# Optimization experiments

Measured on AMD Instinct MI355X. Metric: run time of the kernel, lower is better.

Reference implementation:

```python
import jax, jax.numpy as jnp
import numpy as np

TOP_K_PCT = 0.25   # cfg.dsa_top_k_pct
STRIDE = 8         # hardcoded downsample stride in derive_mask
SIGMOID_SHARP = 10.0
NEG_INF = -1e9


def setup_inputs() -> dict:
    key = jax.random.key(0)
    kq, kk, kv, ku = jax.random.split(key, 4)
    B, nH, T, hd = 1, 4, 4096, 128
    Q = jax.random.normal(kq, (B, nH, T, hd), dtype=jnp.float32)
    K = jax.random.normal(kk, (B, nH, T, hd), dtype=jnp.float32)
    V = jax.random.normal(kv, (B, nH, T, hd), dtype=jnp.float32)
    U = jax.random.uniform(ku, (B, T), dtype=jnp.float32)
    return {"Q": Q, "K": K, "V": V, "U": U}


def _derive_mask(Q, K, U):
    B, nH, T, hd = Q.shape
    scale = hd ** -0.5
    # downsampled local attention scores: (B, nH, T//8, T//8)
    Q_ds = Q[:, :, ::STRIDE, :]
    K_ds = K[:, :, ::STRIDE, :]
    scores = jnp.einsum('bhid,bhjd->bhij', Q_ds, K_ds) * scale
    # upsample back to (B, nH, T, T) via nearest-neighbor repeat
    scores_full = jnp.repeat(jnp.repeat(scores, STRIDE, axis=2), STRIDE, axis=3)[:, :, :T, :T]
    # ECT uncertainty weighting: (B, 1, T, 1)
    u_scale = (1.0 + jnp.clip(U, 0.0, 1.0))[:, None, :, None]
    scores_full = scores_full * u_scale
    # per-row k-th largest value == kthvalue(T - k + 1 smallest)
    k = max(1, int(T * TOP_K_PCT))
    threshold_val = jax.lax.top_k(scores_full, k)[0][..., -1:]  # (B, nH, T, 1)
    return jax.nn.sigmoid((scores_full - threshold_val) * SIGMOID_SHARP)


def reference(Q, K, V, U):
    B, nH, T, hd = Q.shape
    scale = hd ** -0.5
    mask = _derive_mask(Q, K, U)
    causal = jnp.tril(jnp.ones((T, T), dtype=bool))
    mask = mask * causal[None, None, :, :]
    scores = jnp.einsum('bhid,bhjd->bhij', Q, K) * scale
    scores = scores + (1.0 - mask) * NEG_INF
    attn = jax.nn.softmax(scores, axis=-1)
    return jnp.einsum('bhij,bhjd->bhid', attn, V)
```

## Files before the change

### kernel.cpp

```cpp
#include <hip/hip_runtime.h>
#include <math.h>

#define T_SEQ 4096
#define HD 128
#define NH 4
#define DS 512
#define SCALE 0.08838834764831845f
#define NEG9 (-1.0e9f)
#define BN 32
#define NCH 128
#define NRT 256
#define SEG 16
#define TOTSEG2 144
#define NVP 32
#define ALIVE_MIN (-999999936.0f)

typedef __attribute__((ext_vector_type(8))) _Float16 half8;
typedef __attribute__((ext_vector_type(4))) float floatx4;

__device__ __forceinline__ float sigmoidf_(float x) {
  if (x >= 0.0f) return 1.0f / (1.0f + expf(-x));
  float e = expf(x);
  return e / (1.0f + e);
}

#define GLDS16(g, l)                                                  \
  __builtin_amdgcn_global_load_lds(                                   \
      (const __attribute__((address_space(1))) void*)(g),             \
      (__attribute__((address_space(3))) void*)(l), 16, 0, 0)

__global__ __launch_bounds__(256) void prepsds_kernel(
    const float* __restrict__ Q, const float* __restrict__ K, const float* __restrict__ V,
    _Float16* __restrict__ KVb, float* __restrict__ Vpart, float* __restrict__ sds) {
  const int bx = blockIdx.x, tid = threadIdx.x;
  __shared__ float tile[32][133];
  __shared__ float red[2][128];
  __shared__ float Qs[16][132];
  __shared__ float Ks[16][132];
  if (bx < 512) {
    const int hh = bx >> 7, c = bx & 127;
    const int j0 = c * 32;
    const int w = tid >> 6, lane = tid & 63;
    const size_t blob = (size_t)(hh * NCH + c) * 12288;
#pragma unroll
    for (int tt = 0; tt < 2; ++tt) {
      const int t = w + tt * 4;
      const int halfj = t >> 2, dd = t & 3;
      const int q = lane >> 4, jm = lane & 15;
      const float* src =
          &K[(size_t)((hh * T_SEQ) + j0 + halfj * 16 + jm) * HD + dd * 32 + q * 8];
      float4 x0 = *(const float4*)src;
      float4 x1 = *(const float4*)(src + 4);
      float v[8] = {x0.x, x0.y, x0.z, x0.w, x1.x, x1.y, x1.z, x1.w};
      half8 oh, oe;
#pragma unroll
      for (int e = 0; e < 8; ++e) {
        _Float16 hv = (_Float16)v[e];
        oh[e] = hv;
        oe[e] = (_Float16)(v[e] - (float)hv);
      }
      const size_t o = blob + ((size_t)t * 64 + lane) * 8;
      *(half8*)&KVb[o] = oh;
      *(half8*)&KVb[o + 4096] = oe;
    }
    for (int k = 0; k < 4; ++k) {
      int row = (tid >> 5) + k * 8;
      int col = (tid & 31) * 4;
      *(float4*)&tile[row][col] =
          *(const float4*)&V[(size_t)((hh * T_SEQ) + j0 + row) * HD + col];
    }
    __syncthreads();
#pragma unroll
    for (int s2 = 0; s2 < 2; ++s2) {
      const int o8 = tid + s2 * 256;
      const int t2 = o8 >> 6, lane2 = o8 & 63;
      const int qa = lane2 >> 4, dl = lane2 & 15;
      const int col = (t2 >> 1) * 32 + (t2 & 1) * 16 + dl;
      half8 v8;
#pragma unroll
      for (int e = 0; e < 8; ++e) {
        const int row = (e < 4) ? (qa * 4 + e) : (16 + qa * 4 + (e - 4));
        v8[e] = (_Float16)tile[row][col];
      }
      *(half8*)&KVb[blob + 8192 + (size_t)o8 * 8] = v8;
    }
  } else if (bx < 640) {
    int b = bx - 512;
    int hh = b >> 5, part = b & 31;
    int d = tid & 127, hlf = tid >> 7;
    const int j0 = part * 128 + hlf;
    float s0 = 0.f, s1 = 0.f;
    for (int j = j0; j < part * 128 + 128; j += 4) {
      s0 += V[(size_t)((hh * T_SEQ) + j) * HD + d];
      s1 += V[(size_t)((hh * T_SEQ) + j + 2) * HD + d];
    }
    red[hlf][d] = s0 + s1;
    __syncthreads();
    if (tid < 128)
      Vpart[(hh * NVP + part) * 128 + tid] = red[0][tid] + red[1][tid];
  } else {
    int b = bx - 640;
    const int bxs = b & 31, bys = (b >> 5) & 31, hh = b >> 10;
    for (int t = tid; t < 512; t += 256) {
      int r = t >> 5, f = (t & 31) * 4;
      *(float4*)&Qs[r][f] = *(const float4*)&Q[((hh * T_SEQ) + (bys * 16 + r) * 8) * HD + f];
      *(float4*)&Ks[r][f] = *(const float4*)&K[((hh * T_SEQ) + (bxs * 16 + r) * 8) * HD + f];
    }
    __syncthreads();
    const int ty = tid >> 4, tx = tid & 15;
    float acc = 0.0f;
    for (int k = 0; k < 32; ++k) {
      float4 a = *(float4*)&Qs[ty][k * 4];
      float4 bq = *(float4*)&Ks[tx][k * 4];
      acc += a.x * bq.x + a.y * bq.y + a.z * bq.z + a.w * bq.w;
    }
    sds[((hh * DS) + bys * 16 + ty) * DS + bxs * 16 + tx] = acc * SCALE;
  }
}

__global__ __launch_bounds__(256) void bmaxthr_kernel(const float* __restrict__ sds,
                                                      const float* __restrict__ U,
                                                      float* __restrict__ thrG,
                                                      float* __restrict__ bmax16) {
  const int h = blockIdx.y, rt = blockIdx.x;
  const int tid = threadIdx.x, ww = tid >> 6, lane = tid & 63;
  __shared__ float thrS[2];
  if (ww < 2) {
    const int row = h * DS + rt * 2 + ww;
    unsigned v[8];
    for (int t = 0; t < 8; ++t) {
      float f = sds[(size_t)row * DS + t * 64 + lane];
      unsigned b = __float_as_uint(f);
      v[t] = (b & 0x80000000u) ? ~b : (b | 0x80000000u);
    }
    unsigned prefix = 0u;
    for (int bit = 31; bit >= 0; --bit) {
      unsigned cand = prefix | (1u << bit);
      int c = 0;
      for (int t = 0; t < 8; ++t) c += (v[t] >= cand) ? 1 : 0;
      for (int off = 32; off > 0; off >>= 1) c += __shfl_down(c, off, 64);
      c = __shfl(c, 0, 64);
      if (c >= 128) prefix = cand;
    }
    if (lane == 0) {
      unsigned b = (prefix & 0x80000000u) ? (prefix ^ 0x80000000u) : ~prefix;
      float t = __uint_as_float(b);
      thrS[ww] = t;
      thrG[row] = t;
    }
  }
  __syncthreads();
  const int r = lane >> 2, q = lane & 3;
  const int i = rt * 16 + r;
  float u = U[i];
  u = fminf(fmaxf(u, 0.0f), 1.0f);
  const float us = 1.0f + u;
  const int idl = r >> 3;
  const float bb = us * thrS[idl];
  const float* srow = &sds[((h * DS) + rt * 2 + idl) * DS];
  for (int c = ww; c < NCH; c += 4) {
    float sval = srow[(c << 2) + q];
    float a = us * sval;
    float bias = (1.0f - sigmoidf_((a - bb) * 10.0f)) * NEG9;
    for (int off = 1; off < 64; off <<= 1)
      bias = fmaxf(bias, __shfl_xor(bias, off, 64));
    if (lane == 0) bmax16[((h * NRT) + rt) * NCH + c] = bias;
  }
}

__global__ __launch_bounds__(512) void attn128_kernel(
    const float* __restrict__ Qf, const _Float16* __restrict__ KVb,
    const float* __restrict__ U, const float* __restrict__ sds,
    const float* __restrict__ thrG, const float* __restrict__ bmax16,
    float* __restrict__ Pm, float* __restrict__ Pl, _Float16* __restrict__ Po,
    const float* __restrict__ Vpart, float* __restrict__ out) {
  const int h = blockIdx.y;
  const int p = TOTSEG2 - 1 - (int)blockIdx.x;
  int s = 0;
#pragma unroll
  for (int t = 1; t <= 7; ++t)
    if (p >= 32 * t - 2 * t * (t - 1)) s = t;
  const int g = 4 * s + (p - (32 * s - 2 * s * (s - 1)));
  const int seg = s;
  const int cmax = 4 * g + 4;
  const int c0 = seg * SEG;
  const int len = min(SEG, cmax - c0);
  const int nsegG = (cmax + 15) >> 4;

  const int tid = threadIdx.x;
  const int w = tid >> 6;
  const int lane = tid & 63;
  const int quad = lane >> 4;
  const int n = lane & 15;

  const int rt = g * 8 + w;
  const int iw0 = g * 128 + w * 16;
  const int nchW = (rt >> 1) + 1;

  __shared__ __align__(16) _Float16 Sbuf[2][12288];
  __shared__ unsigned uHot[8], uNN[8];
  __shared__ float VsS[128];

  const int myidn = (iw0 >> 3) + (n >> 3);
  float usn, bbn;
  {
    float u = U[iw0 + n];
    u = fminf(fmaxf(u, 0.0f), 1.0f);
    usn = 1.0f + u;
    bbn = usn * thrG[h * DS + myidn];
  }

  half8 qfh[4], qfe[4];
  {
    const float* qrow = &Qf[(size_t)((h * T_SEQ) + iw0 + n) * HD + quad * 8];
#pragma unroll
    for (int d = 0; d < 4; ++d) {
      float4 x0 = *(const float4*)&qrow[d * 32];
      float4 x1 = *(const float4*)&qrow[d * 32 + 4];
      float v[8] = {x0.x, x0.y, x0.z, x0.w, x1.x, x1.y, x1.z, x1.w};
      half8 hh, ee;
#pragma unroll
      for (int t = 0; t < 8; ++t) {
        _Float16 hv = (_Float16)v[t];
        hh[t] = hv;
        ee[t] = (_Float16)(v[t] - (float)hv);
      }
      qfh[d] = hh;
      qfe[d] = ee;
    }
  }
  half8 vones;
#pragma unroll
  for (int e = 0; e < 8; ++e) vones[e] = (_Float16)1.0f;

  floatx4 acc[8];
  for (int t = 0; t < 8; ++t) acc[t] = (floatx4){0.f, 0.f, 0.f, 0.f};
  floatx4 accL = (floatx4){0.f, 0.f, 0.f, 0.f};
  float m_ = -INFINITY;

  float bval = -3.0e38f;
  bool validc = false;
  if (lane < len) {
    int c = c0 + lane;
    validc = (c < nchW);
    bval = bmax16[((h * NRT) + rt) * NCH + c];
  }
  const unsigned bits = (1u << len) - 1u;
  const unsigned myHot = (unsigned)__ballot(lane < len && validc && bval > -124.0f) & bits;
  const unsigned myNull = (unsigned)__ballot(lane < len && (!validc || bval == NEG9)) & bits;
  const unsigned myCold = bits & ~myHot & ~myNull;
  if (lane == 0) { uHot[w] = myHot; uNN[w] = myHot | myCold; }
  __syncthreads();
  unsigned it0 = uHot[0] | uHot[1] | uHot[2] | uHot[3] |
                 uHot[4] | uHot[5] | uHot[6] | uHot[7];
  unsigned it1 = (uNN[0] | uNN[1] | uNN[2] | uNN[3] |
                  uNN[4] | uNN[5] | uNN[6] | uNN[7]) & ~it0;

  const size_t hcbase = (size_t)(h * NCH);
#define STAGE(cc, bsel)                                                          \
  {                                                                              \
    const _Float16* gsrc =                                                       \
        KVb + (hcbase + (size_t)(c0 + (cc))) * 12288 + w * 1536 + lane * 8;      \
    _Float16* ldst = &Sbuf[bsel][w * 1536];                                      \
    GLDS16(gsrc, ldst);                                                          \
    GLDS16(gsrc + 512, ldst + 512);                                              \
    GLDS16(gsrc + 1024, ldst + 1024);                                            \
  }

  int curc = -1;
  if (it0) { curc = __builtin_ctz(it0); it0 &= it0 - 1; }
  else if (it1) { curc = __builtin_ctz(it1); it1 &= it1 - 1; }
  int cur = 0;
  if (curc >= 0) STAGE(curc, 0);

  while (curc >= 0) {
    __syncthreads();
    int nxtc = -1;
    if (it0) { nxtc = __builtin_ctz(it0); it0 &= it0 - 1; }
    else if (it1) { nxtc = __builtin_ctz(it1); it1 &= it1 - 1; }
    if (nxtc >= 0) STAGE(nxtc, cur ^ 1);

    bool run = ((myHot | myCold) >> curc) & 1;
    if (run && ((myCold >> curc) & 1)) {
      float bm16 = __shfl(bval, curc, 64);
      float mm = m_;
      for (int d = 1; d < 16; d <<= 1) mm = fminf(mm, __shfl_xor(mm, d, 64));
      if (bm16 + 12.0f < mm - 40.0f) run = false;
    }
    if (run) {
      const _Float16* Sb = &Sbuf[cur][0];
      const int c = c0 + curc;
      const int j0 = c * BN;

      const int jj = quad >> 1;
      const float sv1 = sds[((h * DS) + myidn) * DS + (c << 2) + jj];
      const float sv2 = sds[((h * DS) + myidn) * DS + (c << 2) + 2 + jj];
      const float bias1 = (1.0f - sigmoidf_((usn * sv1 - bbn) * 10.0f)) * NEG9;
      const float bias2 = (1.0f - sigmoidf_((usn * sv2 - bbn) * 10.0f)) * NEG9;

      half8 kh0[4], kh1[4];
#pragma unroll
      for (int d = 0; d < 4; ++d) {
        kh0[d] = *(const half8*)&Sb[(size_t)(d * 64 + lane) * 8];
        kh1[d] = *(const half8*)&Sb[(size_t)((4 + d) * 64 + lane) * 8];
      }

      floatx4 S0a = (floatx4){0.f, 0.f, 0.f, 0.f};
      floatx4 S0b = (floatx4){0.f, 0.f, 0.f, 0.f};
      floatx4 S1a = (floatx4){0.f, 0.f, 0.f, 0.f};
      floatx4 S1b = (floatx4){0.f, 0.f, 0.f, 0.f};
      S0a = __builtin_amdgcn_mfma_f32_16x16x32_f16(kh0[0], qfh[0], S0a, 0, 0, 0);
      S0b = __builtin_amdgcn_mfma_f32_16x16x32_f16(kh0[2], qfh[2], S0b, 0, 0, 0);
      S1a = __builtin_amdgcn_mfma_f32_16x16x32_f16(kh1[0], qfh[0], S1a, 0, 0, 0);
      S1b = __builtin_amdgcn_mfma_f32_16x16x32_f16(kh1[2], qfh[2], S1b, 0, 0, 0);
      S0a = __builtin_amdgcn_mfma_f32_16x16x32_f16(kh0[1], qfh[1], S0a, 0, 0, 0);
      S0b = __builtin_amdgcn_mfma_f32_16x16x32_f16(kh0[3], qfh[3], S0b, 0, 0, 0);
      S1a = __builtin_amdgcn_mfma_f32_16x16x32_f16(kh1[1], qfh[1], S1a, 0, 0, 0);
      S1b = __builtin_amdgcn_mfma_f32_16x16x32_f16(kh1[3], qfh[3], S1b, 0, 0, 0);

      S0a = __builtin_amdgcn_mfma_f32_16x16x32_f16(kh0[0], qfe[0], S0a, 0, 0, 0);
      S0b = __builtin_amdgcn_mfma_f32_16x16x32_f16(kh0[2], qfe[2], S0b, 0, 0, 0);
      S1a = __builtin_amdgcn_mfma_f32_16x16x32_f16(kh1[0], qfe[0], S1a, 0, 0, 0);
      S1b = __builtin_amdgcn_mfma_f32_16x16x32_f16(kh1[2], qfe[2], S1b, 0, 0, 0);
      S0a = __builtin_amdgcn_mfma_f32_16x16x32_f16(kh0[1], qfe[1], S0a, 0, 0, 0);
      S0b = __builtin_amdgcn_mfma_f32_16x16x32_f16(kh0[3], qfe[3], S0b, 0, 0, 0);
      S1a = __builtin_amdgcn_mfma_f32_16x16x32_f16(kh1[1], qfe[1], S1a, 0, 0, 0);
      S1b = __builtin_amdgcn_mfma_f32_16x16x32_f16(kh1[3], qfe[3], S1b, 0, 0, 0);

      half8 ke0[4], ke1[4];
#pragma unroll
      for (int d = 0; d < 4; ++d) {
        ke0[d] = *(const half8*)&Sb[4096 + (size_t)(d * 64 + lane) * 8];
        ke1[d] = *(const half8*)&Sb[4096 + (size_t)((4 + d) * 64 + lane) * 8];
      }
      S0a = __builtin_amdgcn_mfma_f32_16x16x32_f16(ke0[0], qfh[0], S0a, 0, 0, 0);
      S0b = __builtin_amdgcn_mfma_f32_16x16x32_f16(ke0[2], qfh[2], S0b, 0, 0, 0);
      S1a = __builtin_amdgcn_mfma_f32_16x16x32_f16(ke1[0], qfh[0], S1a, 0, 0, 0);
      S1b = __builtin_amdgcn_mfma_f32_16x16x32_f16(ke1[2], qfh[2], S1b, 0, 0, 0);
      S0a = __builtin_amdgcn_mfma_f32_16x16x32_f16(ke0[1], qfh[1], S0a, 0, 0, 0);
      S0b = __builtin_amdgcn_mfma_f32_16x16x32_f16(ke0[3], qfh[3], S0b, 0, 0, 0);
      S1a = __builtin_amdgcn_mfma_f32_16x16x32_f16(ke1[1], qfh[1], S1a, 0, 0, 0);
      S1b = __builtin_amdgcn_mfma_f32_16x16x32_f16(ke1[3], qfh[3], S1b, 0, 0, 0);

      const floatx4 S0 = S0a + S0b;
      const floatx4 S1 = S1a + S1b;

      const int i = iw0 + n;
      float sc0[4], sc1[4];
      for (int r = 0; r < 4; ++r) {
        const int jA = j0 + quad * 4 + r;
        sc0[r] = (jA <= i) ? (S0[r] * SCALE + bias1) : NEG9;
        sc1[r] = (jA + 16 <= i) ? (S1[r] * SCALE + bias2) : NEG9;
      }

      bool within = true;
      for (int r = 0; r < 4; ++r)
        within = within && (sc0[r] <= m_ + 8.0f) && (sc1[r] <= m_ + 8.0f);
      _Float16 ph0[4], ph1[4];
      if (__all(within)) {
        for (int r = 0; r < 4; ++r) {
          ph0[r] = (_Float16)__expf(sc0[r] - m_);
          ph1[r] = (_Float16)__expf(sc1[r] - m_);
        }
      } else {
        float mx = sc0[0];
        for (int r = 1; r < 4; ++r) mx = fmaxf(mx, sc0[r]);
        for (int r = 0; r < 4; ++r) mx = fmaxf(mx, sc1[r]);
        mx = fmaxf(mx, __shfl_xor(mx, 16, 64));
        mx = fmaxf(mx, __shfl_xor(mx, 32, 64));
        const float mnew = fmaxf(m_, mx);
        const float alpha = __expf(m_ - mnew);
        for (int r = 0; r < 4; ++r) {
          ph0[r] = (_Float16)__expf(sc0[r] - mnew);
          ph1[r] = (_Float16)__expf(sc1[r] - mnew);
        }
        m_ = mnew;
        if (__any(alpha != 1.0f)) {
          float aO[4];
#pragma unroll
          for (int r = 0; r < 4; ++r) aO[r] = __shfl(alpha, quad * 4 + r, 64);
          for (int t = 0; t < 8; ++t)
            for (int r = 0; r < 4; ++r) acc[t][r] *= aO[r];
          for (int r = 0; r < 4; ++r) accL[r] *= aO[r];
        }
      }

      half8 pp;
#pragma unroll
      for (int r = 0; r < 4; ++r) { pp[r] = ph0[r]; pp[4 + r] = ph1[r]; }

      half8 vf[8];
#pragma unroll
      for (int t = 0; t < 8; ++t)
        vf[t] = *(const half8*)&Sb[8192 + (size_t)(t * 64 + lane) * 8];

#pragma unroll
      for (int t = 0; t < 8; ++t)
        acc[t] = __builtin_amdgcn_mfma_f32_16x16x32_f16(pp, vf[t], acc[t], 0, 0, 0);
      accL = __builtin_amdgcn_mfma_f32_16x16x32_f16(pp, vones, accL, 0, 0, 0);
    }
    cur ^= 1;
    curc = nxtc;
  }

  float mrow[4];
#pragma unroll
  for (int r = 0; r < 4; ++r) mrow[r] = __shfl(m_, quad * 4 + r, 64);

  if (nsegG == 1) {
    if (tid < 128) {
      float ss = 0.f;
      for (int pt = 0; pt < NVP; ++pt) ss += Vpart[(h * NVP + pt) * 128 + tid];
      VsS[tid] = ss;
    }
    __syncthreads();
    for (int r = 0; r < 4; ++r) {
      const int row = iw0 + quad * 4 + r;
      const bool dead = (mrow[r] < ALIVE_MIN);
      const float Linv = dead ? 0.0f : 1.0f / accL[r];
#pragma unroll
      for (int t = 0; t < 8; ++t) {
        const int col = t * 16 + n;
        float o = dead ? VsS[col] * 0.000244140625f : acc[t][r] * Linv;
        out[(size_t)((h * T_SEQ) + row) * HD + col] = o;
      }
    }
    return;
  }
  __syncthreads();
  const size_t pbase = (size_t)(h * TOTSEG2 + p);
  if (quad == 0) Pm[pbase * 128 + w * 16 + n] = m_;
  if (n == 0) {
    for (int r = 0; r < 4; ++r)
      Pl[pbase * 128 + w * 16 + quad * 4 + r] = accL[r];
  }
  _Float16* Ob = &Sbuf[0][0];
#pragma unroll
  for (int t = 0; t < 8; ++t)
    for (int r = 0; r < 4; ++r)
      Ob[(size_t)(w * 16 + quad * 4 + r) * 128 + t * 16 + n] = (_Float16)acc[t][r];
  __syncthreads();
  {
    const half8* Os = (const half8*)Ob;
    half8* Pod = (half8*)&Po[pbase * 16384];
    for (int idx = tid; idx < 2048; idx += 512) Pod[idx] = Os[idx];
  }
}

__global__ __launch_bounds__(256) void reduce128_kernel(const float* __restrict__ Pm,
                                                        const float* __restrict__ Pl,
                                                        const _Float16* __restrict__ Po,
                                                        const float* __restrict__ Vpart,
                                                        float* __restrict__ out) {
  const int bx = blockIdx.x;
  const int g = 4 + (bx >> 3);
  const int rb = bx & 7;
  const int h = blockIdx.y;
  const int ns = (g >> 2) + 1;
  const int tid = threadIdx.x;
  const int lr = tid >> 4;
  const int d0 = (tid & 15) * 8;
  const int r = rb * 16 + lr;

  float m[8], M = -INFINITY;
  int pp[8];
#pragma unroll
  for (int ss = 0; ss < 8; ++ss) {
    if (ss < ns) {
      pp[ss] = 32 * ss - 2 * ss * (ss - 1) + g - 4 * ss;
      m[ss] = Pm[(size_t)(h * TOTSEG2 + pp[ss]) * 128 + r];
      M = fmaxf(M, m[ss]);
    }
  }
  const bool dead = (M < ALIVE_MIN);
  float es[8], L = 0.f;
#pragma unroll
  for (int ss = 0; ss < 8; ++ss) {
    if (ss < ns) {
      es[ss] = (dead || m[ss] == -INFINITY) ? 0.0f : expf(m[ss] - M);
      L += Pl[(size_t)(h * TOTSEG2 + pp[ss]) * 128 + r] * es[ss];
    }
  }

  float o[8];
#pragma unroll
  for (int e = 0; e < 8; ++e) o[e] = 0.f;
  if (dead) {
    float4 sa = {0.f, 0.f, 0.f, 0.f}, sb = {0.f, 0.f, 0.f, 0.f};
    for (int pt = 0; pt < NVP; ++pt) {
      const float* vp = &Vpart[(h * NVP + pt) * 128 + d0];
      float4 x0 = *(const float4*)vp;
      float4 x1 = *(const float4*)(vp + 4);
      sa.x += x0.x; sa.y += x0.y; sa.z += x0.z; sa.w += x0.w;
      sb.x += x1.x; sb.y += x1.y; sb.z += x1.z; sb.w += x1.w;
    }
    o[0] = sa.x * 0.000244140625f; o[1] = sa.y * 0.000244140625f;
    o[2] = sa.z * 0.000244140625f; o[3] = sa.w * 0.000244140625f;
    o[4] = sb.x * 0.000244140625f; o[5] = sb.y * 0.000244140625f;
    o[6] = sb.z * 0.000244140625f; o[7] = sb.w * 0.000244140625f;
  } else {
    const float Linv = 1.0f / L;
#pragma unroll
    for (int ss = 0; ss < 8; ++ss) {
      if (ss < ns) {
        half8 v = *(const half8*)&Po[(size_t)(h * TOTSEG2 + pp[ss]) * 16384 + r * 128 + d0];
#pragma unroll
        for (int e = 0; e < 8; ++e) o[e] += (float)v[e] * es[ss];
      }
    }
#pragma unroll
    for (int e = 0; e < 8; ++e) o[e] *= Linv;
  }
  float* dst = &out[(size_t)((h * T_SEQ) + g * 128 + r) * HD + d0];
  float4 w0 = {o[0], o[1], o[2], o[3]};
  float4 w1 = {o[4], o[5], o[6], o[7]};
  *(float4*)dst = w0;
  *(float4*)(dst + 4) = w1;
}

extern "C" void kernel_launch(void* const* d_in, const int* in_sizes, int n_in,
                              void* d_out, int out_size, void* d_ws, size_t ws_size,
                              hipStream_t stream) {
  const float* Q = (const float*)d_in[0];
  const float* K = (const float*)d_in[1];
  const float* V = (const float*)d_in[2];
  const float* U = (const float*)d_in[3];
  float* out = (float*)d_out;

  char* wsb = (char*)d_ws;
  float* sds = (float*)wsb;
  float* thrG = (float*)(wsb + 4194304);
  float* bmax16 = (float*)(wsb + 4202496);
  float* Vpart = (float*)(wsb + 4726784);
  _Float16* KVb = (_Float16*)(wsb + 4792320);
  float* Pm = (float*)(wsb + 17375232);
  float* Pl = (float*)(wsb + 17670144);
  _Float16* Po = (_Float16*)(wsb + 17965056);

  prepsds_kernel<<<4736, 256, 0, stream>>>(Q, K, V, KVb, Vpart, sds);
  bmaxthr_kernel<<<dim3(NRT, NH), 256, 0, stream>>>(sds, U, thrG, bmax16);
  attn128_kernel<<<dim3(TOTSEG2, NH), 512, 0, stream>>>(Q, KVb, U, sds, thrG, bmax16,
                                                        Pm, Pl, Po, Vpart, out);
  reduce128_kernel<<<dim3(224, NH), 256, 0, stream>>>(Pm, Pl, Po, Vpart, out);
}
```

Measured before the change: 224.3 us.

## Process two 16-row tiles per wavefront in attention kernel with 256 threads

The attention kernel now runs 4 wavefronts per block instead of 8, and each wavefront handles two 16-row query tiles. Every K/V fragment read from LDS therefore feeds MFMAs for both tiles, halving LDS fragment traffic per row and giving more independent MFMAs to interleave. The cost is roughly double the accumulator and Q-fragment registers per wave, which may lower occupancy. Each wave also issues twice as many global-to-LDS loads per stage, and the cold-chunk skip test is now shared across both tiles, so it becomes more conservative.

```diff
diff --git a/kernel.cpp b/kernel.cpp
--- a/kernel.cpp
+++ b/kernel.cpp
@@ -168,7 +168,7 @@
   }
 }
 
-__global__ __launch_bounds__(512) void attn128_kernel(
+__global__ __launch_bounds__(256) void attn128_kernel(
     const float* __restrict__ Qf, const _Float16* __restrict__ KVb,
     const float* __restrict__ U, const float* __restrict__ sds,
     const float* __restrict__ thrG, const float* __restrict__ bmax16,
@@ -193,26 +193,27 @@
   const int quad = lane >> 4;
   const int n = lane & 15;
 
-  const int rt = g * 8 + w;
-  const int iw0 = g * 128 + w * 16;
-  const int nchW = (rt >> 1) + 1;
-
   __shared__ __align__(16) _Float16 Sbuf[2][12288];
-  __shared__ unsigned uHot[8], uNN[8];
+  __shared__ unsigned uHot[4], uNN[4];
   __shared__ float VsS[128];
 
-  const int myidn = (iw0 >> 3) + (n >> 3);
-  float usn, bbn;
-  {
-    float u = U[iw0 + n];
+  int iw0t[2], rtt[2], myid[2];
+  float usn[2], bbn[2];
+#pragma unroll
+  for (int tt = 0; tt < 2; ++tt) {
+    iw0t[tt] = g * 128 + (w * 2 + tt) * 16;
+    rtt[tt] = g * 8 + w * 2 + tt;
+    myid[tt] = (iw0t[tt] >> 3) + (n >> 3);
+    float u = U[iw0t[tt] + n];
     u = fminf(fmaxf(u, 0.0f), 1.0f);
-    usn = 1.0f + u;
-    bbn = usn * thrG[h * DS + myidn];
-  }
-
-  half8 qfh[4], qfe[4];
-  {
-    const float* qrow = &Qf[(size_t)((h * T_SEQ) + iw0 + n) * HD + quad * 8];
+    usn[tt] = 1.0f + u;
+    bbn[tt] = usn[tt] * thrG[h * DS + myid[tt]];
+  }
+
+  half8 qfh[2][4], qfe[2][4];
+#pragma unroll
+  for (int tt = 0; tt < 2; ++tt) {
+    const float* qrow = &Qf[(size_t)((h * T_SEQ) + iw0t[tt] + n) * HD + quad * 8];
 #pragma unroll
     for (int d = 0; d < 4; ++d) {
       float4 x0 = *(const float4*)&qrow[d * 32];
@@ -225,46 +226,59 @@
         hh[t] = hv;
         ee[t] = (_Float16)(v[t] - (float)hv);
       }
-      qfh[d] = hh;
-      qfe[d] = ee;
+      qfh[tt][d] = hh;
+      qfe[tt][d] = ee;
     }
   }
   half8 vones;
 #pragma unroll
   for (int e = 0; e < 8; ++e) vones[e] = (_Float16)1.0f;
 
-  floatx4 acc[8];
-  for (int t = 0; t < 8; ++t) acc[t] = (floatx4){0.f, 0.f, 0.f, 0.f};
-  floatx4 accL = (floatx4){0.f, 0.f, 0.f, 0.f};
-  float m_ = -INFINITY;
-
-  float bval = -3.0e38f;
-  bool validc = false;
+  floatx4 acc[2][8];
+#pragma unroll
+  for (int tt = 0; tt < 2; ++tt)
+    for (int t = 0; t < 8; ++t) acc[tt][t] = (floatx4){0.f, 0.f, 0.f, 0.f};
+  floatx4 accL[2];
+  accL[0] = (floatx4){0.f, 0.f, 0.f, 0.f};
+  accL[1] = (floatx4){0.f, 0.f, 0.f, 0.f};
+  float m_[2] = {-INFINITY, -INFINITY};
+
+  float bv[2] = {-3.0e38f, -3.0e38f};
+  bool hot0 = false, hot1 = false, nul0 = true, nul1 = true;
   if (lane < len) {
     int c = c0 + lane;
-    validc = (c < nchW);
-    bval = bmax16[((h * NRT) + rt) * NCH + c];
-  }
+#pragma unroll
+    for (int tt = 0; tt < 2; ++tt) {
+      bool vd = (c < (rtt[tt] >> 1) + 1);
+      float b = bmax16[((h * NRT) + rtt[tt]) * NCH + c];
+      bv[tt] = b;
+      bool ht = vd && b > -124.0f;
+      bool nl = (!vd) || b == NEG9;
+      if (tt == 0) { hot0 = ht; nul0 = nl; } else { hot1 = ht; nul1 = nl; }
+    }
+  }
+  const float bvalM = fmaxf(bv[0], bv[1]);
   const unsigned bits = (1u << len) - 1u;
-  const unsigned myHot = (unsigned)__ballot(lane < len && validc && bval > -124.0f) & bits;
-  const unsigned myNull = (unsigned)__ballot(lane < len && (!validc || bval == NEG9)) & bits;
+  const unsigned myHot = (unsigned)__ballot(lane < len && (hot0 || hot1)) & bits;
+  const unsigned myNull = (unsigned)__ballot(lane < len && nul0 && nul1) & bits;
   const unsigned myCold = bits & ~myHot & ~myNull;
   if (lane == 0) { uHot[w] = myHot; uNN[w] = myHot | myCold; }
   __syncthreads();
-  unsigned it0 = uHot[0] | uHot[1] | uHot[2] | uHot[3] |
-                 uHot[4] | uHot[5] | uHot[6] | uHot[7];
-  unsigned it1 = (uNN[0] | uNN[1] | uNN[2] | uNN[3] |
-                  uNN[4] | uNN[5] | uNN[6] | uNN[7]) & ~it0;
+  unsigned it0 = uHot[0] | uHot[1] | uHot[2] | uHot[3];
+  unsigned it1 = (uNN[0] | uNN[1] | uNN[2] | uNN[3]) & ~it0;
 
   const size_t hcbase = (size_t)(h * NCH);
 #define STAGE(cc, bsel)                                                          \
   {                                                                              \
     const _Float16* gsrc =                                                       \
-        KVb + (hcbase + (size_t)(c0 + (cc))) * 12288 + w * 1536 + lane * 8;      \
-    _Float16* ldst = &Sbuf[bsel][w * 1536];                                      \
+        KVb + (hcbase + (size_t)(c0 + (cc))) * 12288 + w * 3072 + lane * 8;      \
+    _Float16* ldst = &Sbuf[bsel][w * 3072];                                      \
     GLDS16(gsrc, ldst);                                                          \
     GLDS16(gsrc + 512, ldst + 512);                                              \
     GLDS16(gsrc + 1024, ldst + 1024);                                            \
+    GLDS16(gsrc + 1536, ldst + 1536);                                            \
+    GLDS16(gsrc + 2048, ldst + 2048);                                            \
+    GLDS16(gsrc + 2560, ldst + 2560);                                            \
   }
 
   int curc = -1;
@@ -282,8 +296,8 @@
 
     bool run = ((myHot | myCold) >> curc) & 1;
     if (run && ((myCold >> curc) & 1)) {
-      float bm16 = __shfl(bval, curc, 64);
-      float mm = m_;
+      float bm16 = __shfl(bvalM, curc, 64);
+      float mm = fminf(m_[0], m_[1]);
       for (int d = 1; d < 16; d <<= 1) mm = fminf(mm, __shfl_xor(mm, d, 64));
       if (bm16 + 12.0f < mm - 40.0f) run = false;
     }
@@ -291,121 +305,119 @@
       const _Float16* Sb = &Sbuf[cur][0];
       const int c = c0 + curc;
       const int j0 = c * BN;
-
       const int jj = quad >> 1;
-      const float sv1 = sds[((h * DS) + myidn) * DS + (c << 2) + jj];
-      const float sv2 = sds[((h * DS) + myidn) * DS + (c << 2) + 2 + jj];
-      const float bias1 = (1.0f - sigmoidf_((usn * sv1 - bbn) * 10.0f)) * NEG9;
-      const float bias2 = (1.0f - sigmoidf_((usn * sv2 - bbn) * 10.0f)) * NEG9;
-
-      half8 kh0[4], kh1[4];
+
+      float bias1[2], bias2[2];
+#pragma unroll
+      for (int tt = 0; tt < 2; ++tt) {
+        const float sv1 = sds[((h * DS) + myid[tt]) * DS + (c << 2) + jj];
+        const float sv2 = sds[((h * DS) + myid[tt]) * DS + (c << 2) + 2 + jj];
+        bias1[tt] = (1.0f - sigmoidf_((usn[tt] * sv1 - bbn[tt]) * 10.0f)) * NEG9;
+        bias2[tt] = (1.0f - sigmoidf_((usn[tt] * sv2 - bbn[tt]) * 10.0f)) * NEG9;
+      }
+
+      floatx4 S0[2], S1[2];
+      S0[0] = (floatx4){0.f, 0.f, 0.f, 0.f};
+      S0[1] = (floatx4){0.f, 0.f, 0.f, 0.f};
+      S1[0] = (floatx4){0.f, 0.f, 0.f, 0.f};
+      S1[1] = (floatx4){0.f, 0.f, 0.f, 0.f};
 #pragma unroll
       for (int d = 0; d < 4; ++d) {
-        kh0[d] = *(const half8*)&Sb[(size_t)(d * 64 + lane) * 8];
-        kh1[d] = *(const half8*)&Sb[(size_t)((4 + d) * 64 + lane) * 8];
-      }
-
-      floatx4 S0a = (floatx4){0.f, 0.f, 0.f, 0.f};
-      floatx4 S0b = (floatx4){0.f, 0.f, 0.f, 0.f};
-      floatx4 S1a = (floatx4){0.f, 0.f, 0.f, 0.f};
-      floatx4 S1b = (floatx4){0.f, 0.f, 0.f, 0.f};
-      S0a = __builtin_amdgcn_mfma_f32_16x16x32_f16(kh0[0], qfh[0], S0a, 0, 0, 0);
-      S0b = __builtin_amdgcn_mfma_f32_16x16x32_f16(kh0[2], qfh[2], S0b, 0, 0, 0);
-      S1a = __builtin_amdgcn_mfma_f32_16x16x32_f16(kh1[0], qfh[0], S1a, 0, 0, 0);
-      S1b = __builtin_amdgcn_mfma_f32_16x16x32_f16(kh1[2], qfh[2], S1b, 0, 0, 0);
-      S0a = __builtin_amdgcn_mfma_f32_16x16x32_f16(kh0[1], qfh[1], S0a, 0, 0, 0);
-      S0b = __builtin_amdgcn_mfma_f32_16x16x32_f16(kh0[3], qfh[3], S0b, 0, 0, 0);
-      S1a = __builtin_amdgcn_mfma_f32_16x16x32_f16(kh1[1], qfh[1], S1a, 0, 0, 0);
-      S1b = __builtin_amdgcn_mfma_f32_16x16x32_f16(kh1[3], qfh[3], S1b, 0, 0, 0);
-
-      S0a = __builtin_amdgcn_mfma_f32_16x16x32_f16(kh0[0], qfe[0], S0a, 0, 0, 0);
-      S0b = __builtin_amdgcn_mfma_f32_16x16x32_f16(kh0[2], qfe[2], S0b, 0, 0, 0);
-      S1a = __builtin_amdgcn_mfma_f32_16x16x32_f16(kh1[0], qfe[0], S1a, 0, 0, 0);
-      S1b = __builtin_amdgcn_mfma_f32_16x16x32_f16(kh1[2], qfe[2], S1b, 0, 0, 0);
-      S0a = __builtin_amdgcn_mfma_f32_16x16x32_f16(kh0[1], qfe[1], S0a, 0, 0, 0);
-      S0b = __builtin_amdgcn_mfma_f32_16x16x32_f16(kh0[3], qfe[3], S0b, 0, 0, 0);
-      S1a = __builtin_amdgcn_mfma_f32_16x16x32_f16(kh1[1], qfe[1], S1a, 0, 0, 0);
-      S1b = __builtin_amdgcn_mfma_f32_16x16x32_f16(kh1[3], qfe[3], S1b, 0, 0, 0);
-
-      half8 ke0[4], ke1[4];
+        const half8 k0 = *(const half8*)&Sb[(size_t)(d * 64 + lane) * 8];
+        const half8 k1 = *(const half8*)&Sb[(size_t)((4 + d) * 64 + lane) * 8];
+        S0[0] = __builtin_amdgcn_mfma_f32_16x16x32_f16(k0, qfh[0][d], S0[0], 0, 0, 0);
+        S1[0] = __builtin_amdgcn_mfma_f32_16x16x32_f16(k1, qfh[0][d], S1[0], 0, 0, 0);
+        S0[1] = __builtin_amdgcn_mfma_f32_16x16x32_f16(k0, qfh[1][d], S0[1], 0, 0, 0);
+        S1[1] = __builtin_amdgcn_mfma_f32_16x16x32_f16(k1, qfh[1][d], S1[1], 0, 0, 0);
+        S0[0] = __builtin_amdgcn_mfma_f32_16x16x32_f16(k0, qfe[0][d], S0[0], 0, 0, 0);
+        S1[0] = __builtin_amdgcn_mfma_f32_16x16x32_f16(k1, qfe[0][d], S1[0], 0, 0, 0);
+        S0[1] = __builtin_amdgcn_mfma_f32_16x16x32_f16(k0, qfe[1][d], S0[1], 0, 0, 0);
+        S1[1] = __builtin_amdgcn_mfma_f32_16x16x32_f16(k1, qfe[1][d], S1[1], 0, 0, 0);
+      }
 #pragma unroll
       for (int d = 0; d < 4; ++d) {
-        ke0[d] = *(const half8*)&Sb[4096 + (size_t)(d * 64 + lane) * 8];
-        ke1[d] = *(const half8*)&Sb[4096 + (size_t)((4 + d) * 64 + lane) * 8];
-      }
-      S0a = __builtin_amdgcn_mfma_f32_16x16x32_f16(ke0[0], qfh[0], S0a, 0, 0, 0);
-      S0b = __builtin_amdgcn_mfma_f32_16x16x32_f16(ke0[2], qfh[2], S0b, 0, 0, 0);
-      S1a = __builtin_amdgcn_mfma_f32_16x16x32_f16(ke1[0], qfh[0], S1a, 0, 0, 0);
-      S1b = __builtin_amdgcn_mfma_f32_16x16x32_f16(ke1[2], qfh[2], S1b, 0, 0, 0);
-      S0a = __builtin_amdgcn_mfma_f32_16x16x32_f16(ke0[1], qfh[1], S0a, 0, 0, 0);
-      S0b = __builtin_amdgcn_mfma_f32_16x16x32_f16(ke0[3], qfh[3], S0b, 0, 0, 0);
-      S1a = __builtin_amdgcn_mfma_f32_16x16x32_f16(ke1[1], qfh[1], S1a, 0, 0, 0);
-      S1b = __builtin_amdgcn_mfma_f32_16x16x32_f16(ke1[3], qfh[3], S1b, 0, 0, 0);
-
-      const floatx4 S0 = S0a + S0b;
-      const floatx4 S1 = S1a + S1b;
-
-      const int i = iw0 + n;
-      float sc0[4], sc1[4];
+        const half8 e0 = *(const half8*)&Sb[4096 + (size_t)(d * 64 + lane) * 8];
+        const half8 e1 = *(const half8*)&Sb[4096 + (size_t)((4 + d) * 64 + lane) * 8];
+        S0[0] = __builtin_amdgcn_mfma_f32_16x16x32_f16(e0, qfh[0][d], S0[0], 0, 0, 0);
+        S1[0] = __builtin_amdgcn_mfma_f32_16x16x32_f16(e1, qfh[0][d], S1[0], 0, 0, 0);
+        S0[1] = __builtin_amdgcn_mfma_f32_16x16x32_f16(e0, qfh[1][d], S0[1], 0, 0, 0);
+        S1[1] = __builtin_amdgcn_mfma_f32_16x16x32_f16(e1, qfh[1][d], S1[1], 0, 0, 0);
+      }
+
+      float sc0[2][4], sc1[2][4];
+#pragma unroll
+      for (int tt = 0; tt < 2; ++tt) {
+        const int i = iw0t[tt] + n;
+        for (int r = 0; r < 4; ++r) {
+          const int jA = j0 + quad * 4 + r;
+          sc0[tt][r] = (jA <= i) ? (S0[tt][r] * SCALE + bias1[tt]) : NEG9;
+          sc1[tt][r] = (jA + 16 <= i) ? (S1[tt][r] * SCALE + bias2[tt]) : NEG9;
+        }
+      }
+      bool within = true;
+#pragma unroll
+      for (int tt = 0; tt < 2; ++tt)
+        for (int r = 0; r < 4; ++r)
+          within = within && (sc0[tt][r] <= m_[tt] + 8.0f) &&
+                   (sc1[tt][r] <= m_[tt] + 8.0f);
+      _Float16 ph0[2][4], ph1[2][4];
+      if (__all(within)) {
+#pragma unroll
+        for (int tt = 0; tt < 2; ++tt)
+          for (int r = 0; r < 4; ++r) {
+            ph0[tt][r] = (_Float16)__expf(sc0[tt][r] - m_[tt]);
+            ph1[tt][r] = (_Float16)__expf(sc1[tt][r] - m_[tt]);
+          }
+      } else {
+#pragma unroll
+        for (int tt = 0; tt < 2; ++tt) {
+          float mx = sc0[tt][0];
+          for (int r = 1; r < 4; ++r) mx = fmaxf(mx, sc0[tt][r]);
+          for (int r = 0; r < 4; ++r) mx = fmaxf(mx, sc1[tt][r]);
+          mx = fmaxf(mx, __shfl_xor(mx, 16, 64));
+          mx = fmaxf(mx, __shfl_xor(mx, 32, 64));
+          const float mnew = fmaxf(m_[tt], mx);
+          const float alpha = __expf(m_[tt] - mnew);
+          for (int r = 0; r < 4; ++r) {
+            ph0[tt][r] = (_Float16)__expf(sc0[tt][r] - mnew);
+            ph1[tt][r] = (_Float16)__expf(sc1[tt][r] - mnew);
+          }
+          m_[tt] = mnew;
+          if (__any(alpha != 1.0f)) {
+            float aO[4];
+#pragma unroll
+            for (int r = 0; r < 4; ++r) aO[r] = __shfl(alpha, quad * 4 + r, 64);
+            for (int t = 0; t < 8; ++t)
+              for (int r = 0; r < 4; ++r) acc[tt][t][r] *= aO[r];
+            for (int r = 0; r < 4; ++r) accL[tt][r] *= aO[r];
+          }
+        }
+      }
+
+      half8 pp0, pp1;
+#pragma unroll
       for (int r = 0; r < 4; ++r) {
-        const int jA = j0 + quad * 4 + r;
-        sc0[r] = (jA <= i) ? (S0[r] * SCALE + bias1) : NEG9;
-        sc1[r] = (jA + 16 <= i) ? (S1[r] * SCALE + bias2) : NEG9;
-      }
-
-      bool within = true;
-      for (int r = 0; r < 4; ++r)
-        within = within && (sc0[r] <= m_ + 8.0f) && (sc1[r] <= m_ + 8.0f);
-      _Float16 ph0[4], ph1[4];
-      if (__all(within)) {
-        for (int r = 0; r < 4; ++r) {
-          ph0[r] = (_Float16)__expf(sc0[r] - m_);
-          ph1[r] = (_Float16)__expf(sc1[r] - m_);
-        }
-      } else {
-        float mx = sc0[0];
-        for (int r = 1; r < 4; ++r) mx = fmaxf(mx, sc0[r]);
-        for (int r = 0; r < 4; ++r) mx = fmaxf(mx, sc1[r]);
-        mx = fmaxf(mx, __shfl_xor(mx, 16, 64));
-        mx = fmaxf(mx, __shfl_xor(mx, 32, 64));
-        const float mnew = fmaxf(m_, mx);
-        const float alpha = __expf(m_ - mnew);
-        for (int r = 0; r < 4; ++r) {
-          ph0[r] = (_Float16)__expf(sc0[r] - mnew);
-          ph1[r] = (_Float16)__expf(sc1[r] - mnew);
-        }
-        m_ = mnew;
-        if (__any(alpha != 1.0f)) {
-          float aO[4];
-#pragma unroll
-          for (int r = 0; r < 4; ++r) aO[r] = __shfl(alpha, quad * 4 + r, 64);
-          for (int t = 0; t < 8; ++t)
-            for (int r = 0; r < 4; ++r) acc[t][r] *= aO[r];
-          for (int r = 0; r < 4; ++r) accL[r] *= aO[r];
-        }
-      }
-
-      half8 pp;
-#pragma unroll
-      for (int r = 0; r < 4; ++r) { pp[r] = ph0[r]; pp[4 + r] = ph1[r]; }
-
-      half8 vf[8];
-#pragma unroll
-      for (int t = 0; t < 8; ++t)
-        vf[t] = *(const half8*)&Sb[8192 + (size_t)(t * 64 + lane) * 8];
-
-#pragma unroll
-      for (int t = 0; t < 8; ++t)
-        acc[t] = __builtin_amdgcn_mfma_f32_16x16x32_f16(pp, vf[t], acc[t], 0, 0, 0);
-      accL = __builtin_amdgcn_mfma_f32_16x16x32_f16(pp, vones, accL, 0, 0, 0);
+        pp0[r] = ph0[0][r]; pp0[4 + r] = ph1[0][r];
+        pp1[r] = ph0[1][r]; pp1[4 + r] = ph1[1][r];
+      }
+
+#pragma unroll
+      for (int t = 0; t < 8; ++t) {
+        const half8 vf = *(const half8*)&Sb[8192 + (size_t)(t * 64 + lane) * 8];
+        acc[0][t] = __builtin_amdgcn_mfma_f32_16x16x32_f16(pp0, vf, acc[0][t], 0, 0, 0);
+        acc[1][t] = __builtin_amdgcn_mfma_f32_16x16x32_f16(pp1, vf, acc[1][t], 0, 0, 0);
+      }
+      accL[0] = __builtin_amdgcn_mfma_f32_16x16x32_f16(pp0, vones, accL[0], 0, 0, 0);
+      accL[1] = __builtin_amdgcn_mfma_f32_16x16x32_f16(pp1, vones, accL[1], 0, 0, 0);
     }
     cur ^= 1;
     curc = nxtc;
   }
 
-  float mrow[4];
-#pragma unroll
-  for (int r = 0; r < 4; ++r) mrow[r] = __shfl(m_, quad * 4 + r, 64);
+  float mrow[2][4];
+#pragma unroll
+  for (int tt = 0; tt < 2; ++tt)
+    for (int r = 0; r < 4; ++r) mrow[tt][r] = __shfl(m_[tt], quad * 4 + r, 64);
 
   if (nsegG == 1) {
     if (tid < 128) {
@@ -414,36 +426,45 @@
       VsS[tid] = ss;
     }
     __syncthreads();
-    for (int r = 0; r < 4; ++r) {
-      const int row = iw0 + quad * 4 + r;
-      const bool dead = (mrow[r] < ALIVE_MIN);
-      const float Linv = dead ? 0.0f : 1.0f / accL[r];
-#pragma unroll
-      for (int t = 0; t < 8; ++t) {
-        const int col = t * 16 + n;
-        float o = dead ? VsS[col] * 0.000244140625f : acc[t][r] * Linv;
-        out[(size_t)((h * T_SEQ) + row) * HD + col] = o;
-      }
-    }
+#pragma unroll
+    for (int tt = 0; tt < 2; ++tt)
+      for (int r = 0; r < 4; ++r) {
+        const int row = iw0t[tt] + quad * 4 + r;
+        const bool dead = (mrow[tt][r] < ALIVE_MIN);
+        const float Linv = dead ? 0.0f : 1.0f / accL[tt][r];
+#pragma unroll
+        for (int t = 0; t < 8; ++t) {
+          const int col = t * 16 + n;
+          float o = dead ? VsS[col] * 0.000244140625f : acc[tt][t][r] * Linv;
+          out[(size_t)((h * T_SEQ) + row) * HD + col] = o;
+        }
+      }
     return;
   }
   __syncthreads();
   const size_t pbase = (size_t)(h * TOTSEG2 + p);
-  if (quad == 0) Pm[pbase * 128 + w * 16 + n] = m_;
+  if (quad == 0) {
+    Pm[pbase * 128 + (w * 2 + 0) * 16 + n] = m_[0];
+    Pm[pbase * 128 + (w * 2 + 1) * 16 + n] = m_[1];
+  }
   if (n == 0) {
-    for (int r = 0; r < 4; ++r)
-      Pl[pbase * 128 + w * 16 + quad * 4 + r] = accL[r];
+#pragma unroll
+    for (int tt = 0; tt < 2; ++tt)
+      for (int r = 0; r < 4; ++r)
+        Pl[pbase * 128 + (w * 2 + tt) * 16 + quad * 4 + r] = accL[tt][r];
   }
   _Float16* Ob = &Sbuf[0][0];
 #pragma unroll
-  for (int t = 0; t < 8; ++t)
-    for (int r = 0; r < 4; ++r)
-      Ob[(size_t)(w * 16 + quad * 4 + r) * 128 + t * 16 + n] = (_Float16)acc[t][r];
+  for (int tt = 0; tt < 2; ++tt)
+    for (int t = 0; t < 8; ++t)
+      for (int r = 0; r < 4; ++r)
+        Ob[(size_t)((w * 2 + tt) * 16 + quad * 4 + r) * 128 + t * 16 + n] =
+            (_Float16)acc[tt][t][r];
   __syncthreads();
   {
     const half8* Os = (const half8*)Ob;
     half8* Pod = (half8*)&Po[pbase * 16384];
-    for (int idx = tid; idx < 2048; idx += 512) Pod[idx] = Os[idx];
+    for (int idx = tid; idx < 2048; idx += 256) Pod[idx] = Os[idx];
   }
 }
 
@@ -539,7 +560,7 @@
 
   prepsds_kernel<<<4736, 256, 0, stream>>>(Q, K, V, KVb, Vpart, sds);
   bmaxthr_kernel<<<dim3(NRT, NH), 256, 0, stream>>>(sds, U, thrG, bmax16);
-  attn128_kernel<<<dim3(TOTSEG2, NH), 512, 0, stream>>>(Q, KVb, U, sds, thrG, bmax16,
+  attn128_kernel<<<dim3(TOTSEG2, NH), 256, 0, stream>>>(Q, KVb, U, sds, thrG, bmax16,
                                                         Pm, Pl, Po, Vpart, out);
   reduce128_kernel<<<dim3(224, NH), 256, 0, stream>>>(Pm, Pl, Po, Vpart, out);
 }
```

Result: slower. 261.7 us (+16.7%).
